# Kernel optimization log

Hardware: AMD Instinct MI355X
Metric: run time of the kernel (lower is better)

The kernel has to match this reference:

```python
import math
import jax, jax.numpy as jnp
import numpy as np

EMBED = 1024
HIDDEN = 1024
HEADS = 16


def setup_inputs() -> dict:
    key = jax.random.key(0)
    ks = jax.random.split(key, 9)
    B, S = 1, 4096
    s = 1.0 / math.sqrt(EMBED)
    return {
        "x": jax.random.normal(ks[0], (B, S, EMBED), dtype=jnp.float32),
        "Wq": jax.random.normal(ks[1], (EMBED, HIDDEN), dtype=jnp.float32) * s,
        "bq": jnp.zeros((HIDDEN,), dtype=jnp.float32),
        "Wk": jax.random.normal(ks[2], (EMBED, HIDDEN), dtype=jnp.float32) * s,
        "bk": jnp.zeros((HIDDEN,), dtype=jnp.float32),
        "Wv": jax.random.normal(ks[3], (EMBED, HIDDEN), dtype=jnp.float32) * s,
        "bv": jnp.zeros((HIDDEN,), dtype=jnp.float32),
        "Wo": jax.random.normal(ks[4], (EMBED, HIDDEN), dtype=jnp.float32) * s,
        "bo": jnp.zeros((HIDDEN,), dtype=jnp.float32),
    }


def reference(x, Wq, bq, Wk, bk, Wv, bv, Wo, bo):
    B, S, _ = x.shape
    Hd = HIDDEN // HEADS
    # projections: [B,S,hidden] -> [B,H,S,hd]
    def split_heads(t):
        return t.reshape(B, S, HEADS, Hd).transpose(0, 2, 1, 3)
    q = split_heads(x @ Wq + bq)
    k = split_heads(x @ Wk + bk)
    v = split_heads(x @ Wv + bv)
    scale = 1.0 / math.sqrt(EMBED / HEADS)
    scores = jnp.einsum("bhqd,bhkd->bhqk", q, k) * scale  # [B,H,S,S]
    attn = jax.nn.softmax(scores, axis=-1)
    ctx = jnp.einsum("bhqk,bhkd->bhqd", attn, v)
    ctx = ctx.transpose(0, 2, 1, 3).reshape(B, S, HIDDEN)
    return ctx @ Wo + bo
```

## Files before the change

kernel.cpp:

```cpp
#include <hip/hip_runtime.h>
#include <hip/hip_bf16.h>
#include <math.h>

typedef __bf16 bf16;
typedef bf16  bf16x2 __attribute__((ext_vector_type(2)));
typedef bf16  bf16x4 __attribute__((ext_vector_type(4)));
typedef bf16  bf16x8 __attribute__((ext_vector_type(8)));
typedef float f32x4  __attribute__((ext_vector_type(4)));
typedef float f32x16 __attribute__((ext_vector_type(16)));
typedef unsigned uint4v __attribute__((ext_vector_type(4)));

#define MFMA16(a, b, c) __builtin_amdgcn_mfma_f32_16x16x32_bf16((a), (b), (c), 0, 0, 0)
#define MFMA32(a, b, c) __builtin_amdgcn_mfma_f32_32x32x16_bf16((a), (b), (c), 0, 0, 0)

static constexpr int S  = 4096;
static constexpr int E  = 1024;
static constexpr int NH = 16;
static constexpr int HD = 64;

__device__ __forceinline__ void gload16(const bf16* g, bf16* l) {
    __builtin_amdgcn_global_load_lds(
        (const __attribute__((address_space(1))) void*)g,
        (__attribute__((address_space(3))) void*)l, 16, 0, 0);
}

__global__ void convert_f32_bf16(const float* __restrict__ in, bf16* __restrict__ out, int n) {
    int i = (blockIdx.x * blockDim.x + threadIdx.x) * 8;
    if (i < n) {
        float4 v0 = *(const float4*)(in + i);
        float4 v1 = *(const float4*)(in + i + 4);
        bf16x8 o = { (bf16)v0.x, (bf16)v0.y, (bf16)v0.z, (bf16)v0.w,
                     (bf16)v1.x, (bf16)v1.y, (bf16)v1.z, (bf16)v1.w };
        *(bf16x8*)(out + i) = o;
    }
}

__global__ void transpose_w(const float* __restrict__ W0, const float* __restrict__ W1,
                            const float* __restrict__ W2, const float* __restrict__ W3,
                            bf16* __restrict__ T0, bf16* __restrict__ T1,
                            bf16* __restrict__ T2, bf16* __restrict__ T3) {
    const float* W; bf16* T;
    switch (blockIdx.z) {
        case 0: W = W0; T = T0; break;
        case 1: W = W1; T = T1; break;
        case 2: W = W2; T = T2; break;
        default: W = W3; T = T3; break;
    }
    __shared__ float tile[64][65];
    int k0 = blockIdx.x * 64, n0 = blockIdx.y * 64;
    #pragma unroll
    for (int i = 0; i < 16; i++) {
        int idx = threadIdx.x + i * 256;
        int r = idx >> 6, c = idx & 63;
        tile[r][c] = W[(k0 + r) * E + n0 + c];
    }
    __syncthreads();
    #pragma unroll
    for (int i = 0; i < 8; i++) {
        int idx = threadIdx.x + i * 256;
        int r = idx >> 5, c2 = (idx & 31) * 2;
        bf16x2 v = { (bf16)tile[c2][r], (bf16)tile[c2 + 1][r] };
        *(bf16x2*)(T + (n0 + r) * E + k0 + c2) = v;
    }
}

__global__ __launch_bounds__(512) void gemm256_qkv(const bf16* __restrict__ A,
                                                   const bf16* __restrict__ BT,
                                                   const float* __restrict__ b0,
                                                   const float* __restrict__ b1,
                                                   const float* __restrict__ b2,
                                                   bf16* __restrict__ outQ,
                                                   bf16* __restrict__ outK,
                                                   bf16* __restrict__ outV,
                                                   float qscale) {
    extern __shared__ char lds[];
    const int tid = threadIdx.x, lane = tid & 63, w = tid >> 6;
    const int wm = w >> 2, wn = w & 3;
    const int m0 = blockIdx.x * 256, n0 = blockIdx.y * 256;
    const int ln = lane & 15, g = lane >> 4;
    const int swz = (ln & 7) << 4;

    const int sr   = w * 16 + (lane >> 3);
    const int scol = ((lane & 7) ^ ((lane >> 3) & 7)) * 8;
    const bf16* Ag = A  + (size_t)(m0 + sr) * E + scol;
    const bf16* Bg = BT + (size_t)(n0 + sr) * E + scol;

    auto stageT = [&](int buf, int t) {
        const int kc = t * 64;
        #pragma unroll
        for (int hh = 0; hh < 2; hh++)
            #pragma unroll
            for (int j = 0; j < 2; j++)
                gload16(Ag + (size_t)(hh * 128 + j * 8) * E + kc,
                        (bf16*)(lds + (buf * 2 + hh) * 16384 + (w * 16 + j * 8) * 128));
        #pragma unroll
        for (int hh = 0; hh < 2; hh++)
            #pragma unroll
            for (int j = 0; j < 2; j++)
                gload16(Bg + (size_t)(hh * 128 + j * 8) * E + kc,
                        (bf16*)(lds + 65536 + (buf * 2 + hh) * 16384 + (w * 16 + j * 8) * 128));
    };

    f32x4 acc[8][4] = {};
    const int brow = (wn & 1) * 64;
    constexpr int NT = E / 64;

    stageT(0, 0);
    for (int i = 0; i < NT; i++) {
        const int cur = i & 1;
        if (i + 1 < NT) {
            stageT(cur ^ 1, i + 1);
            asm volatile("s_waitcnt vmcnt(8)" ::: "memory");
        } else {
            asm volatile("s_waitcnt vmcnt(0)" ::: "memory");
        }
        __builtin_amdgcn_s_barrier();
        __builtin_amdgcn_sched_barrier(0);

        const char* Ab = lds + (cur * 2 + wm) * 16384;
        const char* Bb = lds + 65536 + (cur * 2 + (wn >> 1)) * 16384;
        #pragma unroll
        for (int kh = 0; kh < 2; kh++) {
            const int cb = kh * 64 + g * 16;
            bf16x8 bfr[4];
            #pragma unroll
            for (int bj = 0; bj < 4; bj++)
                bfr[bj] = *(const bf16x8*)(Bb + (brow + bj * 16 + ln) * 128 + (cb ^ swz));
            __builtin_amdgcn_s_setprio(1);
            #pragma unroll
            for (int mi = 0; mi < 8; mi++) {
                bf16x8 af = *(const bf16x8*)(Ab + (mi * 16 + ln) * 128 + (cb ^ swz));
                #pragma unroll
                for (int bj = 0; bj < 4; bj++)
                    acc[mi][bj] = MFMA16(af, bfr[bj], acc[mi][bj]);
            }
            __builtin_amdgcn_s_setprio(0);
        }
        asm volatile("s_waitcnt lgkmcnt(0)" ::: "memory");
        __builtin_amdgcn_sched_barrier(0);
        __builtin_amdgcn_s_barrier();
    }

    const int proj = n0 >> 10;
    const float* bias = proj == 0 ? b0 : (proj == 1 ? b1 : b2);
    bf16* outp = proj == 0 ? outQ : (proj == 1 ? outK : outV);
    const float osc = proj == 0 ? qscale : 1.0f;
    if (proj < 2) {
        #pragma unroll
        for (int bj = 0; bj < 4; bj++) {
            const int nn = (n0 + wn * 64 + bj * 16 + ln) & 1023;
            const int hh = nn >> 6, dd = nn & 63;
            const float bb = bias[nn];
            #pragma unroll
            for (int mi = 0; mi < 8; mi++) {
                const int m = m0 + wm * 128 + mi * 16 + g * 4;
                #pragma unroll
                for (int r = 0; r < 4; r++)
                    outp[((size_t)hh * S + m + r) * HD + dd] = (bf16)((acc[mi][bj][r] + bb) * osc);
            }
        }
    } else {
        #pragma unroll
        for (int bj = 0; bj < 4; bj++) {
            const int nn = (n0 + wn * 64 + bj * 16 + ln) & 1023;
            const float bb = bias[nn];
            #pragma unroll
            for (int mi = 0; mi < 8; mi++) {
                const int m = m0 + wm * 128 + mi * 16 + g * 4;
                bf16x4 vv = { (bf16)(acc[mi][bj][0] + bb), (bf16)(acc[mi][bj][1] + bb),
                              (bf16)(acc[mi][bj][2] + bb), (bf16)(acc[mi][bj][3] + bb) };
                *(bf16x4*)(outp + (size_t)nn * S + m) = vv;
            }
        }
    }
}

__global__ __launch_bounds__(256) void gemm_o(const bf16* __restrict__ A,
                                              const bf16* __restrict__ BT,
                                              const float* __restrict__ bias,
                                              float* __restrict__ outp) {
    __shared__ __align__(16) bf16 Als[2][128 * 32];
    __shared__ __align__(16) bf16 Bls[2][128 * 32];
    const int tid = threadIdx.x, lane = tid & 63, w = tid >> 6;
    const int wm = w >> 1, wn = w & 1;
    const int m0 = blockIdx.x * 128, n0 = blockIdx.y * 128;
    const int ln = lane & 15, g = lane >> 4;

    const bf16* Ag = A  + (size_t)(m0 + w * 32 + (lane >> 2)) * E + (lane & 3) * 8;
    const bf16* Bg = BT + (size_t)(n0 + w * 32 + (lane >> 2)) * E + (lane & 3) * 8;

    auto stage = [&](int buf, int kt) {
        #pragma unroll
        for (int j = 0; j < 2; j++) {
            gload16(Ag + j * 16 * E + kt, (bf16*)((char*)&Als[buf][0] + w * 2048 + j * 1024));
            gload16(Bg + j * 16 * E + kt, (bf16*)((char*)&Bls[buf][0] + w * 2048 + j * 1024));
        }
    };

    f32x4 acc[4][4] = {};
    stage(0, 0);
    int cur = 0;
    for (int kt = 0; kt < E; kt += 32, cur ^= 1) {
        if (kt + 32 < E) {
            stage(cur ^ 1, kt + 32);
            asm volatile("s_waitcnt vmcnt(4)" ::: "memory");
        } else {
            asm volatile("s_waitcnt vmcnt(0)" ::: "memory");
        }
        __builtin_amdgcn_s_barrier();
        __builtin_amdgcn_sched_barrier(0);

        bf16x8 af[4], bfr[4];
        #pragma unroll
        for (int i = 0; i < 4; i++) {
            af[i]  = *(const bf16x8*)(&Als[cur][0] + (wm * 64 + i * 16 + ln) * 32 + g * 8);
            bfr[i] = *(const bf16x8*)(&Bls[cur][0] + (wn * 64 + i * 16 + ln) * 32 + g * 8);
        }
        __builtin_amdgcn_s_setprio(1);
        #pragma unroll
        for (int mi = 0; mi < 4; mi++)
            #pragma unroll
            for (int bj = 0; bj < 4; bj++)
                acc[mi][bj] = MFMA16(af[mi], bfr[bj], acc[mi][bj]);
        __builtin_amdgcn_s_setprio(0);
        asm volatile("s_waitcnt lgkmcnt(0)" ::: "memory");
        __builtin_amdgcn_sched_barrier(0);
        __builtin_amdgcn_s_barrier();
    }

    #pragma unroll
    for (int bj = 0; bj < 4; bj++) {
        const int n = n0 + wn * 64 + bj * 16 + ln;
        const float bb = bias[n];
        #pragma unroll
        for (int mi = 0; mi < 4; mi++) {
            const int m = m0 + wm * 64 + mi * 16 + g * 4;
            #pragma unroll
            for (int r = 0; r < 4; r++)
                outp[(size_t)(m + r) * E + n] = acc[mi][bj][r] + bb;
        }
    }
}

__global__ __launch_bounds__(512) void flash_attn5(const bf16* __restrict__ Qh,
                                                   const bf16* __restrict__ Kh,
                                                   const bf16* __restrict__ Vt,
                                                   bf16* __restrict__ ctx) {
    __shared__ __align__(16) char smem[65536];
    const int tid = threadIdx.x, lane = tid & 63, w = tid >> 6;
    const int w4 = w & 3, kvh = w >> 2;
    const int h = blockIdx.y, qb = blockIdx.x;
    const int l31 = lane & 31, h5 = lane >> 5;
    const int q_global = qb * 128 + w4 * 32 + l31;

    const bf16* Qbase = Qh + ((size_t)h * S + q_global) * HD;
    bf16x8 qf[4];
    #pragma unroll
    for (int t = 0; t < 4; t++) qf[t] = *(const bf16x8*)(Qbase + t * 16 + h5 * 8);

    const int srow = w4 * 16 + (lane >> 3);
    const int scol = ((lane & 7) ^ (lane >> 3)) * 8;
    const int swz  = (lane & 7) << 4;

    char* const Kb0 = smem + kvh * 16384;
    char* const Vb0 = smem + 32768 + kvh * 16384;

    auto stage = [&](int buf, int kv) {
        #pragma unroll
        for (int j = 0; j < 2; j++) {
            gload16(Kh + ((size_t)h * S + kv + srow + j * 8) * HD + scol,
                    (bf16*)(Kb0 + buf * 8192 + w4 * 2048 + j * 1024));
            gload16(Vt + ((size_t)(h * HD + srow + j * 8)) * S + kv + scol,
                    (bf16*)(Vb0 + buf * 8192 + w4 * 2048 + j * 1024));
        }
    };

    auto exppack = [&](const f32x16& s, bf16x8& pa, bf16x8& pc, float& rs) {
        unsigned d[8];
        #pragma unroll
        for (int i = 0; i < 8; i++) {
            float e0 = __builtin_amdgcn_exp2f(s[2 * i]);
            float e1 = __builtin_amdgcn_exp2f(s[2 * i + 1]);
            rs += e0 + e1;
            asm("v_cvt_pk_bf16_f32 %0, %1, %2" : "=v"(d[i]) : "v"(e0), "v"(e1));
        }
        asm volatile("v_permlane32_swap_b32 %0, %1" : "+v"(d[0]), "+v"(d[2]));
        asm volatile("v_permlane32_swap_b32 %0, %1" : "+v"(d[1]), "+v"(d[3]));
        asm volatile("v_permlane32_swap_b32 %0, %1" : "+v"(d[4]), "+v"(d[6]));
        asm volatile("v_permlane32_swap_b32 %0, %1" : "+v"(d[5]), "+v"(d[7]));
        uint4v fa = { d[0], d[1], d[2], d[3] }, fb = { d[4], d[5], d[6], d[7] };
        pa = __builtin_bit_cast(bf16x8, fa);
        pc = __builtin_bit_cast(bf16x8, fb);
    };

    f32x16 o0 = {}, o1 = {};
    float l_i = 0.f;
    const int kv0 = kvh * (S / 2);
    constexpr int NT = S / 128;

    stage(0, kv0);
    for (int t = 0; t < NT; t++) {
        const int cur = t & 1;
        __syncthreads();
        if (t + 1 < NT) stage(cur ^ 1, kv0 + (t + 1) * 64);

        const char* Kb = Kb0 + cur * 8192;
        const char* Vb = Vb0 + cur * 8192;

        f32x16 s0 = {}, s1 = {};
        __builtin_amdgcn_s_setprio(1);
        #pragma unroll
        for (int t4 = 0; t4 < 4; t4++) {
            const int cb = (t4 * 32 + h5 * 16) ^ swz;
            bf16x8 k0 = *(const bf16x8*)(Kb + l31 * 128 + cb);
            bf16x8 k1 = *(const bf16x8*)(Kb + (32 + l31) * 128 + cb);
            s0 = MFMA32(k0, qf[t4], s0);
            s1 = MFMA32(k1, qf[t4], s1);
        }
        __builtin_amdgcn_s_setprio(0);

        bf16x8 pb[4];
        float rs = 0.f;
        exppack(s0, pb[0], pb[1], rs);
        exppack(s1, pb[2], pb[3], rs);
        l_i += rs;

        __builtin_amdgcn_s_setprio(1);
        #pragma unroll
        for (int ks = 0; ks < 4; ks++) {
            const int cb = (ks * 32 + h5 * 16) ^ swz;
            bf16x8 va  = *(const bf16x8*)(Vb + l31 * 128 + cb);
            bf16x8 vb2 = *(const bf16x8*)(Vb + (32 + l31) * 128 + cb);
            o0 = MFMA32(va, pb[ks], o0);
            o1 = MFMA32(vb2, pb[ks], o1);
        }
        __builtin_amdgcn_s_setprio(0);
    }

    __syncthreads();
    float* const lr  = (float*)(smem + 32768);
    float* const orr = (float*)smem + w4 * 2048;
    if (w >= 4) {
        lr[w4 * 64 + lane] = l_i;
        #pragma unroll
        for (int r = 0; r < 16; r++) orr[r * 64 + lane]        = o0[r];
        #pragma unroll
        for (int r = 0; r < 16; r++) orr[(16 + r) * 64 + lane] = o1[r];
    }
    __syncthreads();
    if (w < 4) {
        l_i += lr[w4 * 64 + lane];
        #pragma unroll
        for (int r = 0; r < 16; r++) o0[r] += orr[r * 64 + lane];
        #pragma unroll
        for (int r = 0; r < 16; r++) o1[r] += orr[(16 + r) * 64 + lane];
        l_i += __shfl_xor(l_i, 32);
        const float inv = 1.f / l_i;
        bf16* cbase = ctx + (size_t)q_global * E + h * HD;
        #pragma unroll
        for (int dg = 0; dg < 2; dg++) {
            const f32x16& o = dg ? o1 : o0;
            #pragma unroll
            for (int rq = 0; rq < 4; rq++) {
                bf16x4 ov = { (bf16)(o[rq * 4 + 0] * inv), (bf16)(o[rq * 4 + 1] * inv),
                              (bf16)(o[rq * 4 + 2] * inv), (bf16)(o[rq * 4 + 3] * inv) };
                *(bf16x4*)(cbase + dg * 32 + rq * 8 + h5 * 4) = ov;
            }
        }
    }
}

extern "C" void kernel_launch(void* const* d_in, const int* in_sizes, int n_in,
                              void* d_out, int out_size, void* d_ws, size_t ws_size,
                              hipStream_t stream) {
    const float* x  = (const float*)d_in[0];
    const float* Wq = (const float*)d_in[1];
    const float* bq = (const float*)d_in[2];
    const float* Wk = (const float*)d_in[3];
    const float* bk = (const float*)d_in[4];
    const float* Wv = (const float*)d_in[5];
    const float* bv = (const float*)d_in[6];
    const float* Wo = (const float*)d_in[7];
    const float* bo = (const float*)d_in[8];

    char* ws = (char*)d_ws;
    const size_t MB = 1u << 20;
    bf16* xb   = (bf16*)(ws + 0 * MB);
    bf16* Wcat = (bf16*)(ws + 8 * MB);
    bf16* tq   = Wcat;
    bf16* tk   = Wcat + 1024 * 1024;
    bf16* tv   = Wcat + 2048 * 1024;
    bf16* to   = (bf16*)(ws + 14 * MB);
    bf16* Qh   = (bf16*)(ws + 16 * MB);
    bf16* Kh   = (bf16*)(ws + 24 * MB);
    bf16* Vt   = (bf16*)(ws + 32 * MB);
    bf16* ctx  = (bf16*)(ws + 40 * MB);

    const float qscale = 0.125f * 1.44269504088896f;

    convert_f32_bf16<<<dim3(S * E / 2048), 256, 0, stream>>>(x, xb, S * E);
    transpose_w<<<dim3(16, 16, 4), 256, 0, stream>>>(Wq, Wk, Wv, Wo, tq, tk, tv, to);

    gemm256_qkv<<<dim3(S / 256, 3072 / 256), 512, 131072, stream>>>(
        xb, Wcat, bq, bk, bv, Qh, Kh, Vt, qscale);

    flash_attn5<<<dim3(S / 128, NH), 512, 0, stream>>>(Qh, Kh, Vt, ctx);

    gemm_o<<<dim3(S / 128, E / 128), 256, 0, stream>>>(ctx, to, bo, (float*)d_out);
}
```

Measured before the change: 147.1 us.

## Merge prep kernels and deepen output GEMM K-tile with swizzled LDS

The activation conversion and weight transpose kernels become one launch, with the block index selecting the role, which removes one kernel launch and its gap. The output projection GEMM doubles its K-tile from 32 to 64, halving the loop iterations and barriers. It also uses an XOR-swizzled LDS layout to avoid bank conflicts on fragment reads. LDS use doubles to 64KB per block, which may reduce occupancy.

New measurement: 144.3 us. Within noise of the previous version (-1.9%).

```diff
diff --git a/kernel.cpp b/kernel.cpp
--- a/kernel.cpp
+++ b/kernel.cpp
@@ -24,30 +24,32 @@
         (__attribute__((address_space(3))) void*)l, 16, 0, 0);
 }
 
-__global__ void convert_f32_bf16(const float* __restrict__ in, bf16* __restrict__ out, int n) {
-    int i = (blockIdx.x * blockDim.x + threadIdx.x) * 8;
-    if (i < n) {
-        float4 v0 = *(const float4*)(in + i);
-        float4 v1 = *(const float4*)(in + i + 4);
+__global__ void prep(const float* __restrict__ x, bf16* __restrict__ xb,
+                     const float* __restrict__ W0, const float* __restrict__ W1,
+                     const float* __restrict__ W2, const float* __restrict__ W3,
+                     bf16* __restrict__ T0, bf16* __restrict__ T1,
+                     bf16* __restrict__ T2, bf16* __restrict__ T3) {
+    const int bid = blockIdx.x;
+    if (bid < 2048) {
+        int i = (bid * 256 + threadIdx.x) * 8;
+        float4 v0 = *(const float4*)(x + i);
+        float4 v1 = *(const float4*)(x + i + 4);
         bf16x8 o = { (bf16)v0.x, (bf16)v0.y, (bf16)v0.z, (bf16)v0.w,
                      (bf16)v1.x, (bf16)v1.y, (bf16)v1.z, (bf16)v1.w };
-        *(bf16x8*)(out + i) = o;
-    }
-}
-
-__global__ void transpose_w(const float* __restrict__ W0, const float* __restrict__ W1,
-                            const float* __restrict__ W2, const float* __restrict__ W3,
-                            bf16* __restrict__ T0, bf16* __restrict__ T1,
-                            bf16* __restrict__ T2, bf16* __restrict__ T3) {
+        *(bf16x8*)(xb + i) = o;
+        return;
+    }
+    const int tb = bid - 2048;
+    const int z = tb >> 8, xy = tb & 255;
+    const int k0 = (xy & 15) * 64, n0 = (xy >> 4) * 64;
     const float* W; bf16* T;
-    switch (blockIdx.z) {
+    switch (z) {
         case 0: W = W0; T = T0; break;
         case 1: W = W1; T = T1; break;
         case 2: W = W2; T = T2; break;
         default: W = W3; T = T3; break;
     }
     __shared__ float tile[64][65];
-    int k0 = blockIdx.x * 64, n0 = blockIdx.y * 64;
     #pragma unroll
     for (int i = 0; i < 16; i++) {
         int idx = threadIdx.x + i * 256;
@@ -175,54 +177,66 @@
     }
 }
 
-__global__ __launch_bounds__(256) void gemm_o(const bf16* __restrict__ A,
-                                              const bf16* __restrict__ BT,
-                                              const float* __restrict__ bias,
-                                              float* __restrict__ outp) {
-    __shared__ __align__(16) bf16 Als[2][128 * 32];
-    __shared__ __align__(16) bf16 Bls[2][128 * 32];
+__global__ __launch_bounds__(256) void gemm_o2(const bf16* __restrict__ A,
+                                               const bf16* __restrict__ BT,
+                                               const float* __restrict__ b0,
+                                               float* __restrict__ outp) {
+    __shared__ __align__(16) bf16 Als[2][128 * 64];
+    __shared__ __align__(16) bf16 Bls[2][128 * 64];
     const int tid = threadIdx.x, lane = tid & 63, w = tid >> 6;
     const int wm = w >> 1, wn = w & 1;
     const int m0 = blockIdx.x * 128, n0 = blockIdx.y * 128;
     const int ln = lane & 15, g = lane >> 4;
-
-    const bf16* Ag = A  + (size_t)(m0 + w * 32 + (lane >> 2)) * E + (lane & 3) * 8;
-    const bf16* Bg = BT + (size_t)(n0 + w * 32 + (lane >> 2)) * E + (lane & 3) * 8;
+    const int swz = (ln & 7) << 4;
+
+    const int scol = ((lane & 7) ^ ((lane >> 3) & 7)) * 8;
+    const bf16* Ag = A  + (size_t)(m0 + w * 32 + (lane >> 3)) * E + scol;
+    const bf16* Bg = BT + (size_t)(n0 + w * 32 + (lane >> 3)) * E + scol;
 
     auto stage = [&](int buf, int kt) {
         #pragma unroll
-        for (int j = 0; j < 2; j++) {
-            gload16(Ag + j * 16 * E + kt, (bf16*)((char*)&Als[buf][0] + w * 2048 + j * 1024));
-            gload16(Bg + j * 16 * E + kt, (bf16*)((char*)&Bls[buf][0] + w * 2048 + j * 1024));
-        }
+        for (int j = 0; j < 4; j++)
+            gload16(Ag + (size_t)j * 8 * E + kt,
+                    (bf16*)((char*)&Als[buf][0] + w * 4096 + j * 1024));
+        #pragma unroll
+        for (int j = 0; j < 4; j++)
+            gload16(Bg + (size_t)j * 8 * E + kt,
+                    (bf16*)((char*)&Bls[buf][0] + w * 4096 + j * 1024));
     };
 
     f32x4 acc[4][4] = {};
+    constexpr int NT = E / 64;
     stage(0, 0);
-    int cur = 0;
-    for (int kt = 0; kt < E; kt += 32, cur ^= 1) {
-        if (kt + 32 < E) {
-            stage(cur ^ 1, kt + 32);
-            asm volatile("s_waitcnt vmcnt(4)" ::: "memory");
+    for (int t = 0; t < NT; t++) {
+        const int cur = t & 1;
+        if (t + 1 < NT) {
+            stage(cur ^ 1, (t + 1) * 64);
+            asm volatile("s_waitcnt vmcnt(8)" ::: "memory");
         } else {
             asm volatile("s_waitcnt vmcnt(0)" ::: "memory");
         }
         __builtin_amdgcn_s_barrier();
         __builtin_amdgcn_sched_barrier(0);
 
-        bf16x8 af[4], bfr[4];
-        #pragma unroll
-        for (int i = 0; i < 4; i++) {
-            af[i]  = *(const bf16x8*)(&Als[cur][0] + (wm * 64 + i * 16 + ln) * 32 + g * 8);
-            bfr[i] = *(const bf16x8*)(&Bls[cur][0] + (wn * 64 + i * 16 + ln) * 32 + g * 8);
-        }
-        __builtin_amdgcn_s_setprio(1);
-        #pragma unroll
-        for (int mi = 0; mi < 4; mi++)
+        const char* Ab = (const char*)&Als[cur][0];
+        const char* Bb = (const char*)&Bls[cur][0];
+        #pragma unroll
+        for (int kh = 0; kh < 2; kh++) {
+            const int cb = kh * 64 + g * 16;
+            bf16x8 bfr[4];
             #pragma unroll
             for (int bj = 0; bj < 4; bj++)
-                acc[mi][bj] = MFMA16(af[mi], bfr[bj], acc[mi][bj]);
-        __builtin_amdgcn_s_setprio(0);
+                bfr[bj] = *(const bf16x8*)(Bb + (wn * 64 + bj * 16 + ln) * 128 + (cb ^ swz));
+            __builtin_amdgcn_s_setprio(1);
+            #pragma unroll
+            for (int mi = 0; mi < 4; mi++) {
+                bf16x8 af = *(const bf16x8*)(Ab + (wm * 64 + mi * 16 + ln) * 128 + (cb ^ swz));
+                #pragma unroll
+                for (int bj = 0; bj < 4; bj++)
+                    acc[mi][bj] = MFMA16(af, bfr[bj], acc[mi][bj]);
+            }
+            __builtin_amdgcn_s_setprio(0);
+        }
         asm volatile("s_waitcnt lgkmcnt(0)" ::: "memory");
         __builtin_amdgcn_sched_barrier(0);
         __builtin_amdgcn_s_barrier();
@@ -231,7 +245,7 @@
     #pragma unroll
     for (int bj = 0; bj < 4; bj++) {
         const int n = n0 + wn * 64 + bj * 16 + ln;
-        const float bb = bias[n];
+        const float bb = b0[n];
         #pragma unroll
         for (int mi = 0; mi < 4; mi++) {
             const int m = m0 + wm * 64 + mi * 16 + g * 4;
@@ -398,13 +412,12 @@
 
     const float qscale = 0.125f * 1.44269504088896f;
 
-    convert_f32_bf16<<<dim3(S * E / 2048), 256, 0, stream>>>(x, xb, S * E);
-    transpose_w<<<dim3(16, 16, 4), 256, 0, stream>>>(Wq, Wk, Wv, Wo, tq, tk, tv, to);
+    prep<<<dim3(3072), 256, 0, stream>>>(x, xb, Wq, Wk, Wv, Wo, tq, tk, tv, to);
 
     gemm256_qkv<<<dim3(S / 256, 3072 / 256), 512, 131072, stream>>>(
         xb, Wcat, bq, bk, bv, Qh, Kh, Vt, qscale);
 
     flash_attn5<<<dim3(S / 128, NH), 512, 0, stream>>>(Qh, Kh, Vt, ctx);
 
-    gemm_o<<<dim3(S / 128, E / 128), 256, 0, stream>>>(ctx, to, bo, (float*)d_out);
-}
+    gemm_o2<<<dim3(S / 128, E / 128), 256, 0, stream>>>(ctx, to, bo, (float*)d_out);
+}
```
